# Kernel optimization log

Hardware: AMD Instinct MI355X
Metric: run time of the kernel (lower is better)

## Reference

```python
import math
import jax, jax.numpy as jnp
import numpy as np

FEATURE_DIM = 16
HEADS = 8
DIM = 512
HEAD_DIM = DIM // HEADS
EPS = 1e-12
_RD = math.sqrt(FEATURE_DIM)        # sqrt(d)
_RRD = math.sqrt(_RD)               # d^{1/4}
_R2 = math.sqrt(2.0)
_IU, _JU = np.triu_indices(FEATURE_DIM, k=1)  # row-major upper-tri (excl diag), matches torch.triu_indices


def taylor_feature_map(x):
    # x: (..., F) -> (..., 1 + F + F + F*(F-1)/2) = (..., 153) for F=16
    off = x[..., _IU] * x[..., _JU]          # upper triangle of outer product, no full FxF materialization
    diag = x * x
    return jnp.concatenate([
        jnp.ones_like(x[..., :1]),
        x / _RRD,
        diag / (_RD * _R2),
        off / _RD,
    ], axis=-1)


def setup_inputs() -> dict:
    key = jax.random.key(0)
    k0, k1, k2, k3, k4 = jax.random.split(key, 5)
    b, t, d = 2, 1024, DIM
    hidden_states = jax.random.normal(k0, (b, t, d), dtype=jnp.float32)
    s = 0.02
    Wq = jax.random.normal(k1, (HEADS * FEATURE_DIM, d), dtype=jnp.float32) * s
    Wk = jax.random.normal(k2, (HEADS * FEATURE_DIM, d), dtype=jnp.float32) * s
    Wv = jax.random.normal(k3, (HEADS * HEAD_DIM, d), dtype=jnp.float32) * s
    Wo = jax.random.normal(k4, (d, HEADS * HEAD_DIM), dtype=jnp.float32) * s
    return {"hidden_states": hidden_states, "Wq": Wq, "Wk": Wk, "Wv": Wv, "Wo": Wo}


def reference(hidden_states, Wq, Wk, Wv, Wo):
    b, t, d = hidden_states.shape
    h, f, hd = HEADS, FEATURE_DIM, HEAD_DIM
    q = (hidden_states @ Wq.T).reshape(b, t, h, f).transpose(0, 2, 1, 3)    # (b,h,t,f)
    k = (hidden_states @ Wk.T).reshape(b, t, h, f).transpose(0, 2, 1, 3)
    v = (hidden_states @ Wv.T).reshape(b, t, h, hd).transpose(0, 2, 1, 3)   # (b,h,t,hd)
    q = taylor_feature_map(q)   # (b,h,t,F) with F=153
    k = taylor_feature_map(k)
    # causal linear attention via cumulative state
    kv = k[..., None, :] * v[..., :, None]          # (b,h,t,hd,F)
    kv_cum = jnp.cumsum(kv, axis=2)                 # (b,h,t,hd,F)
    num = jnp.einsum('bhtf,bhtdf->bhtd', q, kv_cum) # (b,h,t,hd)
    k_cum = jnp.cumsum(k, axis=2)                   # (b,h,t,F)
    den = jnp.einsum('bhtf,bhtf->bht', q, k_cum)[..., None] + EPS
    y = num / den                                   # (b,h,t,hd)
    y = y.transpose(0, 2, 1, 3).reshape(b, t, h * hd)
    return y @ Wo.T
```

## Files before the change

kernel.cpp:

```cpp
#include <hip/hip_runtime.h>
#include <hip/hip_bf16.h>

#define BB 2
#define TT 1024
#define DD 512
#define HH 8
#define FF 16
#define HDIM 64
#define BT (BB*TT)

typedef short bf16x8 __attribute__((ext_vector_type(8)));
typedef float f32x4  __attribute__((ext_vector_type(4)));
#define MFMA_BF16 __builtin_amdgcn_mfma_f32_16x16x32_bf16

__device__ __forceinline__ ushort f2b(float f) {
    uint u = __float_as_uint(f);
    uint r = (u + 0x7fffu + ((u >> 16) & 1u)) >> 16;
    return (ushort)r;
}

__device__ __forceinline__ uint pkbf2(float a, float b) {
    __hip_bfloat162 h = __float22bfloat162_rn(make_float2(a, b));
    union { __hip_bfloat162 h2; uint u; } c; c.h2 = h;
    return c.u;
}

__global__ __launch_bounds__(512) void qkv_f32(
    const float* __restrict__ X,  const float* __restrict__ Wq,
    const float* __restrict__ Wk, const float* __restrict__ Wv,
    const float* __restrict__ Wo,
    ushort* __restrict__ Qb, ushort* __restrict__ Kb,
    ushort* __restrict__ Vtg, ushort* __restrict__ Wob)
{
    if (blockIdx.y == 6) {
        const int idx = blockIdx.x * 512 + threadIdx.x;
        #pragma unroll
        for (int j = 0; j < 8; ++j) {
            const int u = j * 8192 + idx;
            float4 v = *(const float4*)(Wo + (size_t)u * 4);
            ushort4 o = { f2b(v.x), f2b(v.y), f2b(v.z), f2b(v.w) };
            *(ushort4*)(Wob + (size_t)u * 4) = o;
        }
        return;
    }

    __shared__ short LA[128][136];
    __shared__ short LB[128][136];

    const int m0 = blockIdx.x * 128;
    const int by = blockIdx.y;
    const int tid = threadIdx.x, w = tid >> 6, l = tid & 63;
    const int mw = w & 3, nw = w >> 2;
    const int lr = l & 15, g = l >> 4;

    const float* Wsrc = (by == 0) ? Wq
                      : (by == 1) ? Wk
                      : (Wv + (size_t)(by - 2) * 128 * 512);

    f32x4 acc[2][4] = {};

    for (int kc = 0; kc < 4; ++kc) {
        __syncthreads();
        #pragma unroll
        for (int i = 0; i < 8; ++i) {
            const int f = i * 512 + tid;
            const int row = f >> 5, c4 = f & 31;
            float4 va = *(const float4*)(X + (size_t)(m0 + row) * 512 + kc*128 + c4*4);
            uint2 pa = { pkbf2(va.x, va.y), pkbf2(va.z, va.w) };
            *(uint2*)&LA[row][c4*4] = pa;
            float4 vb = *(const float4*)(Wsrc + (size_t)row * 512 + kc*128 + c4*4);
            uint2 pb = { pkbf2(vb.x, vb.y), pkbf2(vb.z, vb.w) };
            *(uint2*)&LB[row][c4*4] = pb;
        }
        __syncthreads();

        #pragma unroll
        for (int ks = 0; ks < 4; ++ks) {
            bf16x8 a0 = *(const bf16x8*)&LA[mw*32      + lr][ks*32 + g*8];
            bf16x8 a1 = *(const bf16x8*)&LA[mw*32 + 16 + lr][ks*32 + g*8];
            bf16x8 b0 = *(const bf16x8*)&LB[nw*64      + lr][ks*32 + g*8];
            bf16x8 b1 = *(const bf16x8*)&LB[nw*64 + 16 + lr][ks*32 + g*8];
            bf16x8 b2 = *(const bf16x8*)&LB[nw*64 + 32 + lr][ks*32 + g*8];
            bf16x8 b3 = *(const bf16x8*)&LB[nw*64 + 48 + lr][ks*32 + g*8];
            acc[0][0] = MFMA_BF16(a0, b0, acc[0][0], 0, 0, 0);
            acc[0][1] = MFMA_BF16(a0, b1, acc[0][1], 0, 0, 0);
            acc[0][2] = MFMA_BF16(a0, b2, acc[0][2], 0, 0, 0);
            acc[0][3] = MFMA_BF16(a0, b3, acc[0][3], 0, 0, 0);
            acc[1][0] = MFMA_BF16(a1, b0, acc[1][0], 0, 0, 0);
            acc[1][1] = MFMA_BF16(a1, b1, acc[1][1], 0, 0, 0);
            acc[1][2] = MFMA_BF16(a1, b2, acc[1][2], 0, 0, 0);
            acc[1][3] = MFMA_BF16(a1, b3, acc[1][3], 0, 0, 0);
        }
    }

    if (by < 2) {
        ushort* Dst = (by == 0) ? Qb : Kb;
        const float scale = (by == 0) ? 1.0f : 0.25f;
        #pragma unroll
        for (int mb = 0; mb < 2; ++mb)
            #pragma unroll
            for (int nb = 0; nb < 4; ++nb) {
                const int n = nw*64 + nb*16 + lr;
                const int h = n >> 4, fc = n & 15;
                #pragma unroll
                for (int r = 0; r < 4; ++r) {
                    const int tok = m0 + mw*32 + mb*16 + g*4 + r;
                    const int b = tok >> 10, tt = tok & 1023;
                    Dst[((size_t)(b*HH + h)*TT + tt)*FF + fc] =
                        f2b(acc[mb][nb][r] * scale);
                }
            }
    } else {
        #pragma unroll
        for (int mb = 0; mb < 2; ++mb)
            #pragma unroll
            for (int nb = 0; nb < 4; ++nb) {
                const int n = (by - 2)*128 + nw*64 + nb*16 + lr;
                const int h = n >> 6, v = n & 63;
                const int tok0 = m0 + mw*32 + mb*16 + g*4;
                const int b = tok0 >> 10, tt0 = tok0 & 1023;
                uint2 pk = { pkbf2(acc[mb][nb][0], acc[mb][nb][1]),
                             pkbf2(acc[mb][nb][2], acc[mb][nb][3]) };
                *(uint2*)&Vtg[((size_t)(b*HH + h)*64 + v)*TT + tt0] = pk;
            }
    }
}

__global__ __launch_bounds__(512) void attn_mfma(
    const ushort* __restrict__ Qb, const ushort* __restrict__ Kb,
    const ushort* __restrict__ Vtg, ushort* __restrict__ Yb)
{
    __shared__ float smem[8*32*68 + 8*32];
    short (*Pl)[32][72] = (short(*)[32][72])smem;
    float* scf = smem;
    float* scd = smem + 8*32*68;

    const int bid = blockIdx.x;
    const int qt = 31 - (bid >> 4);
    const int bh = bid & 15;
    const int b = bh >> 3, h = bh & 7;
    const int tid = threadIdx.x, w = tid >> 6, l = tid & 63;
    const int lr = l & 15, g = l >> 4;
    const int qend = qt*32 + 32;
    const int nkc = (qt + 2) >> 1;
    const bf16x8 zf = {0,0,0,0,0,0,0,0};
    const bf16x8 ones = {16256,16256,16256,16256,16256,16256,16256,16256};

    bf16x8 qf[2];
    #pragma unroll
    for (int nb = 0; nb < 2; ++nb)
        qf[nb] = (l < 32)
            ? *(const bf16x8*)(Qb + ((size_t)bh*TT + qt*32 + nb*16 + lr)*FF + g*8)
            : zf;

    f32x4 o[4][2] = {};
    f32x4 dacc[2] = {};

    for (int kc = w; kc < nkc; kc += 8) {
        const bool diagc = (kc == nkc - 1);
        const int act = qend - kc*64;
        const int nmb = diagc ? (act >> 4) : 4;
        const int kb_max = nmb >> 1;

        for (int mb = 0; mb < nmb; ++mb) {
            bf16x8 kf = (l < 32)
                ? *(const bf16x8*)(Kb + ((size_t)bh*TT + kc*64 + mb*16 + lr)*FF + g*8)
                : zf;
            #pragma unroll
            for (int nb = 0; nb < 2; ++nb) {
                f32x4 z4 = {};
                f32x4 s = MFMA_BF16(kf, qf[nb], z4, 0, 0, 0);
                float pv[4];
                if (diagc) {
                    const int qg = qt*32 + nb*16 + lr;
                    const int kg0 = kc*64 + mb*16 + g*4;
                    #pragma unroll
                    for (int r = 0; r < 4; ++r) {
                        float pp = fmaf(s[r], fmaf(s[r], 0.5f, 1.0f), 1.0f);
                        pv[r] = (kg0 + r > qg) ? 0.f : pp;
                    }
                } else {
                    #pragma unroll
                    for (int r = 0; r < 4; ++r)
                        pv[r] = fmaf(s[r], fmaf(s[r], 0.5f, 1.0f), 1.0f);
                }
                uint2 pk = { pkbf2(pv[0], pv[1]), pkbf2(pv[2], pv[3]) };
                *(uint2*)&Pl[w][nb*16 + lr][mb*16 + g*4] = pk;
            }
        }

        for (int kb = 0; kb < kb_max; ++kb) {
            #pragma unroll
            for (int mv = 0; mv < 4; ++mv) {
                bf16x8 vf = *(const bf16x8*)(Vtg +
                    ((size_t)bh*64 + mv*16 + lr)*TT + kc*64 + kb*32 + g*8);
                #pragma unroll
                for (int nb = 0; nb < 2; ++nb) {
                    bf16x8 pf = *(const bf16x8*)&Pl[w][nb*16 + lr][kb*32 + g*8];
                    o[mv][nb] = MFMA_BF16(vf, pf, o[mv][nb], 0, 0, 0);
                }
            }
            #pragma unroll
            for (int nb = 0; nb < 2; ++nb) {
                bf16x8 pf = *(const bf16x8*)&Pl[w][nb*16 + lr][kb*32 + g*8];
                dacc[nb] = MFMA_BF16(ones, pf, dacc[nb], 0, 0, 0);
            }
        }
    }

    __syncthreads();

    #pragma unroll
    for (int mv = 0; mv < 4; ++mv)
        #pragma unroll
        for (int nb = 0; nb < 2; ++nb)
            *(f32x4*)&scf[(size_t)(w*32 + nb*16 + lr)*68 + mv*16 + g*4] = o[mv][nb];
    if (g == 0) {
        scd[w*32 + lr]      = dacc[0][0];
        scd[w*32 + 16 + lr] = dacc[1][0];
    }

    __syncthreads();

    {
        const int q  = tid >> 4;
        const int v0 = (tid & 15) * 4;
        float dtot = 0.f;
        #pragma unroll
        for (int ww = 0; ww < 8; ++ww) dtot += scd[ww*32 + q];
        const float inv = 1.0f / (dtot + 1e-12f);
        float o0 = 0.f, o1 = 0.f, o2 = 0.f, o3 = 0.f;
        #pragma unroll
        for (int ww = 0; ww < 8; ++ww) {
            const float* p = &scf[(size_t)(ww*32 + q)*68 + v0];
            o0 += p[0]; o1 += p[1]; o2 += p[2]; o3 += p[3];
        }
        uint2 pk = { pkbf2(o0*inv, o1*inv), pkbf2(o2*inv, o3*inv) };
        *(uint2*)(Yb + ((size_t)(b*TT + qt*32 + q))*DD + h*HDIM + v0) = pk;
    }
}

__global__ __launch_bounds__(512) void out_mfma(
    const ushort* __restrict__ Yb, const ushort* __restrict__ Wob,
    float* __restrict__ Out)
{
    __shared__ float sc[2][64][66];
    const int m0 = blockIdx.x * 64, n0 = blockIdx.y * 64;
    const int tid = threadIdx.x, w = tid >> 6, l = tid & 63;
    const int kw = w >> 2, mw = w & 1, nw = (w >> 1) & 1;
    const int lr = l & 15, g = l >> 4;

    f32x4 acc[2][2] = {};
    const ushort* Ar = Yb  + (size_t)(m0 + mw*32 + lr) * 512 + kw*256 + g*8;
    const ushort* Br = Wob + (size_t)(n0 + nw*32 + lr) * 512 + kw*256 + g*8;

    bf16x8 a0c = *(const bf16x8*)(Ar);
    bf16x8 a1c = *(const bf16x8*)(Ar + (size_t)16*512);
    bf16x8 b0c = *(const bf16x8*)(Br);
    bf16x8 b1c = *(const bf16x8*)(Br + (size_t)16*512);
    #pragma unroll
    for (int ks = 0; ks < 8; ++ks) {
        bf16x8 a0n = a0c, a1n = a1c, b0n = b0c, b1n = b1c;
        if (ks < 7) {
            a0n = *(const bf16x8*)(Ar + (ks+1)*32);
            a1n = *(const bf16x8*)(Ar + (size_t)16*512 + (ks+1)*32);
            b0n = *(const bf16x8*)(Br + (ks+1)*32);
            b1n = *(const bf16x8*)(Br + (size_t)16*512 + (ks+1)*32);
        }
        acc[0][0] = MFMA_BF16(a0c, b0c, acc[0][0], 0, 0, 0);
        acc[0][1] = MFMA_BF16(a0c, b1c, acc[0][1], 0, 0, 0);
        acc[1][0] = MFMA_BF16(a1c, b0c, acc[1][0], 0, 0, 0);
        acc[1][1] = MFMA_BF16(a1c, b1c, acc[1][1], 0, 0, 0);
        a0c = a0n; a1c = a1n; b0c = b0n; b1c = b1n;
    }

    #pragma unroll
    for (int mb = 0; mb < 2; ++mb)
        #pragma unroll
        for (int nb = 0; nb < 2; ++nb)
            #pragma unroll
            for (int r = 0; r < 4; ++r)
                sc[kw][mw*32 + mb*16 + g*4 + r][nw*32 + nb*16 + lr] = acc[mb][nb][r];
    __syncthreads();

    const int vl = tid & 63, rg = tid >> 6;
    #pragma unroll
    for (int j = 0; j < 8; ++j) {
        const float v = sc[0][rg*8 + j][vl] + sc[1][rg*8 + j][vl];
        Out[(size_t)(m0 + rg*8 + j)*512 + n0 + vl] = v;
    }
}

extern "C" void kernel_launch(void* const* d_in, const int* in_sizes, int n_in,
                              void* d_out, int out_size, void* d_ws, size_t ws_size,
                              hipStream_t stream) {
    const float* X  = (const float*)d_in[0];
    const float* Wq = (const float*)d_in[1];
    const float* Wk = (const float*)d_in[2];
    const float* Wv = (const float*)d_in[3];
    const float* Wo = (const float*)d_in[4];
    float* out = (float*)d_out;

    ushort* ws = (ushort*)d_ws;
    ushort* Wob = ws;
    ushort* Qb  = Wob + 262144;
    ushort* Kb  = Qb  + 262144;
    ushort* Vtg = Kb  + 262144;
    ushort* Yb  = Vtg + 1048576;

    dim3 g1(16, 7);
    qkv_f32<<<g1, 512, 0, stream>>>(X, Wq, Wk, Wv, Wo, Qb, Kb, Vtg, Wob);

    attn_mfma<<<512, 512, 0, stream>>>(Qb, Kb, Vtg, Yb);

    dim3 g3(BT/64, DD/64);
    out_mfma<<<g3, 512, 0, stream>>>(Yb, Wob, out);
}
```

Measured before the change: 43.07 us.

## Fuse attention and output projection with an XCD-aware grid barrier

Merges the attention kernel and the output-projection GEMM into one persistent launch. A hierarchical grid-wide barrier sits between the two phases: blocks count arrivals per XCD, one leader per XCD waits for all 512 blocks, and leaders then sync across XCDs. This removes one kernel launch and its tail gap. The projection is re-tiled into 32x64 output tiles with a 4-way K split and a reduction in LDS. The risks are deadlock if not all 512 blocks are resident at once, an added memset launch, and barrier spin overhead.

```diff
diff --git a/kernel.cpp b/kernel.cpp
--- a/kernel.cpp
+++ b/kernel.cpp
@@ -23,6 +23,12 @@
     __hip_bfloat162 h = __float22bfloat162_rn(make_float2(a, b));
     union { __hip_bfloat162 h2; uint u; } c; c.h2 = h;
     return c.u;
+}
+
+__device__ __forceinline__ uint get_xcc() {
+    uint x;
+    asm volatile("s_getreg_b32 %0, hwreg(HW_REG_XCC_ID)" : "=s"(x));
+    return x & 7u;
 }
 
 __global__ __launch_bounds__(512) void qkv_f32(
@@ -126,168 +132,203 @@
     }
 }
 
-__global__ __launch_bounds__(512) void attn_mfma(
+__global__ __launch_bounds__(512) void attn_out(
     const ushort* __restrict__ Qb, const ushort* __restrict__ Kb,
-    const ushort* __restrict__ Vtg, ushort* __restrict__ Yb)
+    const ushort* __restrict__ Vtg, const ushort* __restrict__ Wob,
+    ushort* __restrict__ Yb, float* __restrict__ Out,
+    unsigned long long* __restrict__ Bar)
 {
     __shared__ float smem[8*32*68 + 8*32];
     short (*Pl)[32][72] = (short(*)[32][72])smem;
     float* scf = smem;
     float* scd = smem + 8*32*68;
 
+    unsigned long long* B = Bar;
+    uint* S = (uint*)(Bar + 144);
+
     const int bid = blockIdx.x;
-    const int qt = 31 - (bid >> 4);
-    const int bh = bid & 15;
-    const int b = bh >> 3, h = bh & 7;
     const int tid = threadIdx.x, w = tid >> 6, l = tid & 63;
     const int lr = l & 15, g = l >> 4;
-    const int qend = qt*32 + 32;
-    const int nkc = (qt + 2) >> 1;
-    const bf16x8 zf = {0,0,0,0,0,0,0,0};
-    const bf16x8 ones = {16256,16256,16256,16256,16256,16256,16256,16256};
-
-    bf16x8 qf[2];
-    #pragma unroll
-    for (int nb = 0; nb < 2; ++nb)
-        qf[nb] = (l < 32)
-            ? *(const bf16x8*)(Qb + ((size_t)bh*TT + qt*32 + nb*16 + lr)*FF + g*8)
-            : zf;
-
-    f32x4 o[4][2] = {};
-    f32x4 dacc[2] = {};
-
-    for (int kc = w; kc < nkc; kc += 8) {
-        const bool diagc = (kc == nkc - 1);
-        const int act = qend - kc*64;
-        const int nmb = diagc ? (act >> 4) : 4;
-        const int kb_max = nmb >> 1;
-
-        for (int mb = 0; mb < nmb; ++mb) {
-            bf16x8 kf = (l < 32)
-                ? *(const bf16x8*)(Kb + ((size_t)bh*TT + kc*64 + mb*16 + lr)*FF + g*8)
+    const uint xcd = get_xcc();
+
+    if (tid == 0) {
+        if (atomicCAS(&S[xcd], 0u, 1u) == 0u) {
+            unsigned long long r = atomicAdd(&B[4], 1ull);
+            asm volatile("" :: "v"((uint)r));
+        }
+    }
+
+    {
+        const int qt = 31 - (bid >> 4);
+        const int bh = bid & 15;
+        const int b = bh >> 3, h = bh & 7;
+        const int qend = qt*32 + 32;
+        const int nkc = (qt + 2) >> 1;
+        const bf16x8 zf = {0,0,0,0,0,0,0,0};
+        const bf16x8 ones = {16256,16256,16256,16256,16256,16256,16256,16256};
+
+        bf16x8 qf[2];
+        #pragma unroll
+        for (int nb = 0; nb < 2; ++nb)
+            qf[nb] = (l < 32)
+                ? *(const bf16x8*)(Qb + ((size_t)bh*TT + qt*32 + nb*16 + lr)*FF + g*8)
                 : zf;
-            #pragma unroll
-            for (int nb = 0; nb < 2; ++nb) {
-                f32x4 z4 = {};
-                f32x4 s = MFMA_BF16(kf, qf[nb], z4, 0, 0, 0);
-                float pv[4];
-                if (diagc) {
-                    const int qg = qt*32 + nb*16 + lr;
-                    const int kg0 = kc*64 + mb*16 + g*4;
+
+        f32x4 o[4][2] = {};
+        f32x4 dacc[2] = {};
+
+        for (int kc = w; kc < nkc; kc += 8) {
+            const bool diagc = (kc == nkc - 1);
+            const int act = qend - kc*64;
+            const int nmb = diagc ? (act >> 4) : 4;
+            const int kb_max = nmb >> 1;
+
+            for (int mb = 0; mb < nmb; ++mb) {
+                bf16x8 kf = (l < 32)
+                    ? *(const bf16x8*)(Kb + ((size_t)bh*TT + kc*64 + mb*16 + lr)*FF + g*8)
+                    : zf;
+                #pragma unroll
+                for (int nb = 0; nb < 2; ++nb) {
+                    f32x4 z4 = {};
+                    f32x4 s = MFMA_BF16(kf, qf[nb], z4, 0, 0, 0);
+                    float pv[4];
+                    if (diagc) {
+                        const int qg = qt*32 + nb*16 + lr;
+                        const int kg0 = kc*64 + mb*16 + g*4;
+                        #pragma unroll
+                        for (int r = 0; r < 4; ++r) {
+                            float pp = fmaf(s[r], fmaf(s[r], 0.5f, 1.0f), 1.0f);
+                            pv[r] = (kg0 + r > qg) ? 0.f : pp;
+                        }
+                    } else {
+                        #pragma unroll
+                        for (int r = 0; r < 4; ++r)
+                            pv[r] = fmaf(s[r], fmaf(s[r], 0.5f, 1.0f), 1.0f);
+                    }
+                    uint2 pk = { pkbf2(pv[0], pv[1]), pkbf2(pv[2], pv[3]) };
+                    *(uint2*)&Pl[w][nb*16 + lr][mb*16 + g*4] = pk;
+                }
+            }
+
+            for (int kb = 0; kb < kb_max; ++kb) {
+                #pragma unroll
+                for (int mv = 0; mv < 4; ++mv) {
+                    bf16x8 vf = *(const bf16x8*)(Vtg +
+                        ((size_t)bh*64 + mv*16 + lr)*TT + kc*64 + kb*32 + g*8);
                     #pragma unroll
-                    for (int r = 0; r < 4; ++r) {
-                        float pp = fmaf(s[r], fmaf(s[r], 0.5f, 1.0f), 1.0f);
-                        pv[r] = (kg0 + r > qg) ? 0.f : pp;
+                    for (int nb = 0; nb < 2; ++nb) {
+                        bf16x8 pf = *(const bf16x8*)&Pl[w][nb*16 + lr][kb*32 + g*8];
+                        o[mv][nb] = MFMA_BF16(vf, pf, o[mv][nb], 0, 0, 0);
                     }
-                } else {
-                    #pragma unroll
-                    for (int r = 0; r < 4; ++r)
-                        pv[r] = fmaf(s[r], fmaf(s[r], 0.5f, 1.0f), 1.0f);
                 }
-                uint2 pk = { pkbf2(pv[0], pv[1]), pkbf2(pv[2], pv[3]) };
-                *(uint2*)&Pl[w][nb*16 + lr][mb*16 + g*4] = pk;
-            }
-        }
-
-        for (int kb = 0; kb < kb_max; ++kb) {
-            #pragma unroll
-            for (int mv = 0; mv < 4; ++mv) {
-                bf16x8 vf = *(const bf16x8*)(Vtg +
-                    ((size_t)bh*64 + mv*16 + lr)*TT + kc*64 + kb*32 + g*8);
                 #pragma unroll
                 for (int nb = 0; nb < 2; ++nb) {
                     bf16x8 pf = *(const bf16x8*)&Pl[w][nb*16 + lr][kb*32 + g*8];
-                    o[mv][nb] = MFMA_BF16(vf, pf, o[mv][nb], 0, 0, 0);
+                    dacc[nb] = MFMA_BF16(ones, pf, dacc[nb], 0, 0, 0);
                 }
             }
-            #pragma unroll
-            for (int nb = 0; nb < 2; ++nb) {
-                bf16x8 pf = *(const bf16x8*)&Pl[w][nb*16 + lr][kb*32 + g*8];
-                dacc[nb] = MFMA_BF16(ones, pf, dacc[nb], 0, 0, 0);
-            }
+        }
+
+        __syncthreads();
+
+        #pragma unroll
+        for (int mv = 0; mv < 4; ++mv)
+            #pragma unroll
+            for (int nb = 0; nb < 2; ++nb)
+                *(f32x4*)&scf[(size_t)(w*32 + nb*16 + lr)*68 + mv*16 + g*4] = o[mv][nb];
+        if (g == 0) {
+            scd[w*32 + lr]      = dacc[0][0];
+            scd[w*32 + 16 + lr] = dacc[1][0];
+        }
+
+        __syncthreads();
+
+        {
+            const int q  = tid >> 4;
+            const int v0 = (tid & 15) * 4;
+            float dtot = 0.f;
+            #pragma unroll
+            for (int ww = 0; ww < 8; ++ww) dtot += scd[ww*32 + q];
+            const float inv = 1.0f / (dtot + 1e-12f);
+            float o0 = 0.f, o1 = 0.f, o2 = 0.f, o3 = 0.f;
+            #pragma unroll
+            for (int ww = 0; ww < 8; ++ww) {
+                const float* p = &scf[(size_t)(ww*32 + q)*68 + v0];
+                o0 += p[0]; o1 += p[1]; o2 += p[2]; o3 += p[3];
+            }
+            uint2 pk = { pkbf2(o0*inv, o1*inv), pkbf2(o2*inv, o3*inv) };
+            *(uint2*)(Yb + ((size_t)(b*TT + qt*32 + q))*DD + h*HDIM + v0) = pk;
         }
     }
 
     __syncthreads();
-
-    #pragma unroll
-    for (int mv = 0; mv < 4; ++mv)
-        #pragma unroll
-        for (int nb = 0; nb < 2; ++nb)
-            *(f32x4*)&scf[(size_t)(w*32 + nb*16 + lr)*68 + mv*16 + g*4] = o[mv][nb];
-    if (g == 0) {
-        scd[w*32 + lr]      = dacc[0][0];
-        scd[w*32 + 16 + lr] = dacc[1][0];
-    }
-
+    if (tid == 0) {
+        atomicAdd(&B[80 + (size_t)xcd * 8], 1ull);
+        if (atomicCAS(&S[8 + xcd], 0u, 1u) == 0u) {
+            for (;;) {
+                unsigned long long ssum = 0;
+                #pragma unroll
+                for (int x = 0; x < 8; ++x)
+                    ssum += __hip_atomic_load(&B[80 + (size_t)x * 8],
+                                              __ATOMIC_RELAXED,
+                                              __HIP_MEMORY_SCOPE_SYSTEM);
+                if (ssum >= 512ull) break;
+                __builtin_amdgcn_s_sleep(2);
+            }
+            const unsigned long long NX =
+                __hip_atomic_load(&B[4], __ATOMIC_RELAXED,
+                                  __HIP_MEMORY_SCOPE_SYSTEM);
+            __threadfence();
+            atomicAdd(&B[1], 1ull);
+            while (__hip_atomic_load(&B[1], __ATOMIC_RELAXED,
+                                     __HIP_MEMORY_SCOPE_SYSTEM) < NX)
+                __builtin_amdgcn_s_sleep(2);
+            __hip_atomic_store(&B[8 + (size_t)xcd * 8], 1ull,
+                               __ATOMIC_RELAXED, __HIP_MEMORY_SCOPE_SYSTEM);
+        }
+        while (__hip_atomic_load(&B[8 + (size_t)xcd * 8], __ATOMIC_RELAXED,
+                                 __HIP_MEMORY_SCOPE_SYSTEM) < 1ull)
+            __builtin_amdgcn_s_sleep(2);
+    }
     __syncthreads();
 
     {
-        const int q  = tid >> 4;
-        const int v0 = (tid & 15) * 4;
-        float dtot = 0.f;
-        #pragma unroll
-        for (int ww = 0; ww < 8; ++ww) dtot += scd[ww*32 + q];
-        const float inv = 1.0f / (dtot + 1e-12f);
-        float o0 = 0.f, o1 = 0.f, o2 = 0.f, o3 = 0.f;
-        #pragma unroll
-        for (int ww = 0; ww < 8; ++ww) {
-            const float* p = &scf[(size_t)(ww*32 + q)*68 + v0];
-            o0 += p[0]; o1 += p[1]; o2 += p[2]; o3 += p[3];
-        }
-        uint2 pk = { pkbf2(o0*inv, o1*inv), pkbf2(o2*inv, o3*inv) };
-        *(uint2*)(Yb + ((size_t)(b*TT + qt*32 + q))*DD + h*HDIM + v0) = pk;
-    }
-}
-
-__global__ __launch_bounds__(512) void out_mfma(
-    const ushort* __restrict__ Yb, const ushort* __restrict__ Wob,
-    float* __restrict__ Out)
-{
-    __shared__ float sc[2][64][66];
-    const int m0 = blockIdx.x * 64, n0 = blockIdx.y * 64;
-    const int tid = threadIdx.x, w = tid >> 6, l = tid & 63;
-    const int kw = w >> 2, mw = w & 1, nw = (w >> 1) & 1;
-    const int lr = l & 15, g = l >> 4;
-
-    f32x4 acc[2][2] = {};
-    const ushort* Ar = Yb  + (size_t)(m0 + mw*32 + lr) * 512 + kw*256 + g*8;
-    const ushort* Br = Wob + (size_t)(n0 + nw*32 + lr) * 512 + kw*256 + g*8;
-
-    bf16x8 a0c = *(const bf16x8*)(Ar);
-    bf16x8 a1c = *(const bf16x8*)(Ar + (size_t)16*512);
-    bf16x8 b0c = *(const bf16x8*)(Br);
-    bf16x8 b1c = *(const bf16x8*)(Br + (size_t)16*512);
-    #pragma unroll
-    for (int ks = 0; ks < 8; ++ks) {
-        bf16x8 a0n = a0c, a1n = a1c, b0n = b0c, b1n = b1c;
-        if (ks < 7) {
-            a0n = *(const bf16x8*)(Ar + (ks+1)*32);
-            a1n = *(const bf16x8*)(Ar + (size_t)16*512 + (ks+1)*32);
-            b0n = *(const bf16x8*)(Br + (ks+1)*32);
-            b1n = *(const bf16x8*)(Br + (size_t)16*512 + (ks+1)*32);
-        }
-        acc[0][0] = MFMA_BF16(a0c, b0c, acc[0][0], 0, 0, 0);
-        acc[0][1] = MFMA_BF16(a0c, b1c, acc[0][1], 0, 0, 0);
-        acc[1][0] = MFMA_BF16(a1c, b0c, acc[1][0], 0, 0, 0);
-        acc[1][1] = MFMA_BF16(a1c, b1c, acc[1][1], 0, 0, 0);
-        a0c = a0n; a1c = a1n; b0c = b0n; b1c = b1n;
-    }
-
-    #pragma unroll
-    for (int mb = 0; mb < 2; ++mb)
-        #pragma unroll
-        for (int nb = 0; nb < 2; ++nb)
-            #pragma unroll
-            for (int r = 0; r < 4; ++r)
-                sc[kw][mw*32 + mb*16 + g*4 + r][nw*32 + nb*16 + lr] = acc[mb][nb][r];
-    __syncthreads();
-
-    const int vl = tid & 63, rg = tid >> 6;
-    #pragma unroll
-    for (int j = 0; j < 8; ++j) {
-        const float v = sc[0][rg*8 + j][vl] + sc[1][rg*8 + j][vl];
-        Out[(size_t)(m0 + rg*8 + j)*512 + n0 + vl] = v;
+        float (*sc)[32][66] = (float(*)[32][66])smem;
+        const int m0 = (bid >> 3) * 32, n0 = (bid & 7) * 64;
+        const int nw = w & 1, kw = w >> 1;
+
+        f32x4 acc[2][2] = {};
+        const ushort* Ar = Yb  + (size_t)(m0 + lr) * 512 + kw*128 + g*8;
+        const ushort* Br = Wob + (size_t)(n0 + nw*32 + lr) * 512 + kw*128 + g*8;
+
+        #pragma unroll
+        for (int ks = 0; ks < 4; ++ks) {
+            bf16x8 a0 = *(const bf16x8*)(Ar + ks*32);
+            bf16x8 a1 = *(const bf16x8*)(Ar + (size_t)16*512 + ks*32);
+            bf16x8 b0 = *(const bf16x8*)(Br + ks*32);
+            bf16x8 b1 = *(const bf16x8*)(Br + (size_t)16*512 + ks*32);
+            acc[0][0] = MFMA_BF16(a0, b0, acc[0][0], 0, 0, 0);
+            acc[0][1] = MFMA_BF16(a0, b1, acc[0][1], 0, 0, 0);
+            acc[1][0] = MFMA_BF16(a1, b0, acc[1][0], 0, 0, 0);
+            acc[1][1] = MFMA_BF16(a1, b1, acc[1][1], 0, 0, 0);
+        }
+
+        #pragma unroll
+        for (int mb = 0; mb < 2; ++mb)
+            #pragma unroll
+            for (int nb = 0; nb < 2; ++nb)
+                #pragma unroll
+                for (int r = 0; r < 4; ++r)
+                    sc[kw][mb*16 + g*4 + r][nw*32 + nb*16 + lr] = acc[mb][nb][r];
+        __syncthreads();
+
+        const int row = tid >> 4, c0 = (tid & 15) * 4;
+        float4 v;
+        v.x = sc[0][row][c0+0] + sc[1][row][c0+0] + sc[2][row][c0+0] + sc[3][row][c0+0];
+        v.y = sc[0][row][c0+1] + sc[1][row][c0+1] + sc[2][row][c0+1] + sc[3][row][c0+1];
+        v.z = sc[0][row][c0+2] + sc[1][row][c0+2] + sc[2][row][c0+2] + sc[3][row][c0+2];
+        v.w = sc[0][row][c0+3] + sc[1][row][c0+3] + sc[2][row][c0+3] + sc[3][row][c0+3];
+        *(float4*)(Out + (size_t)(m0 + row)*512 + n0 + c0) = v;
     }
 }
 
@@ -307,12 +348,12 @@
     ushort* Kb  = Qb  + 262144;
     ushort* Vtg = Kb  + 262144;
     ushort* Yb  = Vtg + 1048576;
+    unsigned long long* Bar = (unsigned long long*)(ws + 2883584);
+
+    hipMemsetAsync((void*)Bar, 0, 1280, stream);
 
     dim3 g1(16, 7);
     qkv_f32<<<g1, 512, 0, stream>>>(X, Wq, Wk, Wv, Wo, Qb, Kb, Vtg, Wob);
 
-    attn_mfma<<<512, 512, 0, stream>>>(Qb, Kb, Vtg, Yb);
-
-    dim3 g3(BT/64, DD/64);
-    out_mfma<<<g3, 512, 0, stream>>>(Yb, Wob, out);
-}
+    attn_out<<<512, 512, 0, stream>>>(Qb, Kb, Vtg, Wob, Yb, out, Bar);
+}
```

After: 65.27 us. +51.5%, slower.
